# Performance work log

Hardware: AMD Instinct MI355X
Metric: run time of the kernel (lower is better)

## Reference

```python
import jax, jax.numpy as jnp
import numpy as np

N_KNOTS = 16
DEGREE = 3
N_BASES = N_KNOTS - DEGREE - 1  # 12
F_CH = 128
KNOTS = jnp.linspace(0.0, 2.0, N_KNOTS, dtype=jnp.float32)


def bspline_basis(x, knots, degree):
    """Cox-de Boor B-spline basis. x: [...], returns [..., K-degree-1]."""
    K = knots.shape[0]
    xe = x[..., None]
    # degree-0 indicator basis: [..., K-1]
    b = ((xe >= knots[:-1]) & (xe < knots[1:])).astype(x.dtype)
    for d in range(1, degree + 1):
        left_den = knots[d:K - 1] - knots[:K - d - 1]
        right_den = knots[d + 1:K] - knots[1:K - d]
        safe_l = jnp.where(left_den > 0, left_den, 1.0)
        safe_r = jnp.where(right_den > 0, right_den, 1.0)
        left = jnp.where(left_den > 0, (xe - knots[:K - d - 1]) / safe_l, 0.0)
        right = jnp.where(right_den > 0, (knots[d + 1:K] - xe) / safe_r, 0.0)
        b = left * b[..., :K - d - 1] + right * b[..., 1:K - d]
    return b  # [..., K-degree-1]


def setup_inputs() -> dict:
    key = jax.random.key(0)
    k1, k2, k3 = jax.random.split(key, 3)
    B, N = 32, 8192
    eval_x = jax.random.normal(k1, (B, N, F_CH), dtype=jnp.float32)
    eval_eigs = jax.random.uniform(k2, (B, N), dtype=jnp.float32)  # in [0,1) within knot span [0,2]
    filter_scale = 1.0
    filter_coeffs = jax.random.normal(k3, (N_BASES, F_CH), dtype=jnp.float32) * filter_scale
    return {"eval_x": eval_x, "eval_eigs": eval_eigs, "filter_coeffs": filter_coeffs}


def reference(eval_x, eval_eigs, filter_coeffs):
    # basis: [B, N, n_bases]
    basis = bspline_basis(eval_eigs, KNOTS, DEGREE)
    # The torch split/cat/bmm/stack/transpose chain is exactly this contraction:
    # spectral_filter[b,n,f] = sum_k basis[b,n,k] * coeffs[k,f]
    spectral_filter = jnp.einsum('bnk,kf->bnf', basis, filter_coeffs)
    return eval_x * jnp.square(spectral_filter)
```

## Files before the change

### kernel.cpp

```cpp
#include <hip/hip_runtime.h>


#define N_BASES 12
#define F_CH 128
#define CHUNKS 4
#define PAD 3
#define TAB_ROWS (N_BASES + 2 * PAD)
#define ROW_VF4 (F_CH / 4)

typedef float vf4 __attribute__((ext_vector_type(4)));

template <bool EXACT>
__global__ __launch_bounds__(256) void spline_filter_kernel(
    const vf4* __restrict__ x4,
    const float* __restrict__ eigs,
    const vf4* __restrict__ coeffs4,
    vf4*       __restrict__ out4,
    int total4, int stride4)
{
    __shared__ vf4 sc[TAB_ROWS * ROW_VF4];

    const int t = threadIdx.x;
    for (int r = t; r < TAB_ROWS * ROW_VF4; r += 256) {
        const int k = (r >> 5) - PAD;
        sc[r] = ((unsigned)k < (unsigned)N_BASES)
                    ? coeffs4[k * ROW_VF4 + (r & 31)]
                    : (vf4)0.0f;
    }
    __syncthreads();

    const int gid = blockIdx.x * 256 + t;

    float eg[CHUNKS];
    vf4   xv[CHUNKS];

    #pragma unroll
    for (int c = 0; c < CHUNKS; ++c) {
        const int idx = gid + c * stride4;
        if (EXACT || idx < total4) eg[c] = eigs[idx >> 5];
        else                       eg[c] = 0.0f;
    }
    #pragma unroll
    for (int c = 0; c < CHUNKS; ++c) {
        const int idx = gid + c * stride4;
        if (EXACT || idx < total4) xv[c] = __builtin_nontemporal_load(&x4[idx]);
        else                       xv[c] = (vf4)0.0f;
    }

    const int lane = gid & 31;

    #pragma unroll
    for (int c = 0; c < CHUNKS; ++c) {
        const int idx = gid + c * stride4;
        if (!EXACT && idx >= total4) continue;

        const float u = eg[c] * 7.5f;
        int i = (int)u;
        i = min(max(i, 0), N_BASES + 2);
        float tt = u - (float)i;
        tt = fminf(fmaxf(tt, 0.0f), 1.0f);
        const float t2  = tt * tt;
        const float t3  = t2 * tt;
        const float omt = 1.0f - tt;
        const float w0 = omt * omt * omt * (1.0f / 6.0f);
        const float w1 = (3.0f * t3 - 6.0f * t2 + 4.0f) * (1.0f / 6.0f);
        const float w2 = (-3.0f * t3 + 3.0f * t2 + 3.0f * tt + 1.0f) * (1.0f / 6.0f);
        const float w3 = t3 * (1.0f / 6.0f);

        const vf4* row = &sc[i * ROW_VF4 + lane];
        vf4 sf = w0 * row[0]
               + w1 * row[ROW_VF4]
               + w2 * row[2 * ROW_VF4]
               + w3 * row[3 * ROW_VF4];

        const vf4 o = xv[c] * sf * sf;
        __builtin_nontemporal_store(o, &out4[idx]);
    }
}

extern "C" void kernel_launch(void* const* d_in, const int* in_sizes, int n_in,
                              void* d_out, int out_size, void* d_ws, size_t ws_size,
                              hipStream_t stream) {
    const float* eval_x = (const float*)d_in[0];
    const float* eigs   = (const float*)d_in[1];
    const float* coeffs = (const float*)d_in[2];
    float* out = (float*)d_out;

    const int total4  = in_sizes[0] / 4;
    const int blocks  = (total4 + 256 * CHUNKS - 1) / (256 * CHUNKS);
    const int stride4 = blocks * 256;
    const bool exact  = (blocks * 256 * CHUNKS == total4);

    if (exact) {
        spline_filter_kernel<true><<<blocks, 256, 0, stream>>>(
            (const vf4*)eval_x, eigs, (const vf4*)coeffs, (vf4*)out,
            total4, stride4);
    } else {
        spline_filter_kernel<false><<<blocks, 256, 0, stream>>>(
            (const vf4*)eval_x, eigs, (const vf4*)coeffs, (vf4*)out,
            total4, stride4);
    }
}
```

Before: 227.9 us.

## Drop shared-memory coefficient table, read coefficients via cache with clamped indices

Removes the per-block shared-memory staging of the padded coefficient table and its barrier. Each thread now reads the four needed coefficient rows straight from global memory (served by L1/L2), clamping out-of-range basis indices and zeroing their weights. CHUNKS drops from 4 to 2, which doubles the block count, and launch bounds now request 8 blocks per CU for occupancy. The trade is more global/cache loads per element and less memory-level parallelism per thread, in exchange for no LDS setup or sync per block.

After: 226.1 us. Within noise of the previous version (-0.8%).

```diff
diff --git a/kernel.cpp b/kernel.cpp
--- a/kernel.cpp
+++ b/kernel.cpp
@@ -3,33 +3,20 @@
 
 #define N_BASES 12
 #define F_CH 128
-#define CHUNKS 4
-#define PAD 3
-#define TAB_ROWS (N_BASES + 2 * PAD)
+#define CHUNKS 2
 #define ROW_VF4 (F_CH / 4)
 
 typedef float vf4 __attribute__((ext_vector_type(4)));
 
 template <bool EXACT>
-__global__ __launch_bounds__(256) void spline_filter_kernel(
+__global__ __launch_bounds__(256, 8) void spline_filter_kernel(
     const vf4* __restrict__ x4,
     const float* __restrict__ eigs,
     const vf4* __restrict__ coeffs4,
     vf4*       __restrict__ out4,
     int total4, int stride4)
 {
-    __shared__ vf4 sc[TAB_ROWS * ROW_VF4];
-
-    const int t = threadIdx.x;
-    for (int r = t; r < TAB_ROWS * ROW_VF4; r += 256) {
-        const int k = (r >> 5) - PAD;
-        sc[r] = ((unsigned)k < (unsigned)N_BASES)
-                    ? coeffs4[k * ROW_VF4 + (r & 31)]
-                    : (vf4)0.0f;
-    }
-    __syncthreads();
-
-    const int gid = blockIdx.x * 256 + t;
+    const int gid = blockIdx.x * 256 + threadIdx.x;
 
     float eg[CHUNKS];
     vf4   xv[CHUNKS];
@@ -54,24 +41,27 @@
         const int idx = gid + c * stride4;
         if (!EXACT && idx >= total4) continue;
 
-        const float u = eg[c] * 7.5f;
-        int i = (int)u;
-        i = min(max(i, 0), N_BASES + 2);
-        float tt = u - (float)i;
-        tt = fminf(fmaxf(tt, 0.0f), 1.0f);
+        float u = eg[c] * 7.5f;
+        u = fminf(fmaxf(u, 0.0f), 15.0f);
+        const int   i  = (int)u;
+        const float tt = u - (float)i;
         const float t2  = tt * tt;
         const float t3  = t2 * tt;
         const float omt = 1.0f - tt;
-        const float w0 = omt * omt * omt * (1.0f / 6.0f);
-        const float w1 = (3.0f * t3 - 6.0f * t2 + 4.0f) * (1.0f / 6.0f);
-        const float w2 = (-3.0f * t3 + 3.0f * t2 + 3.0f * tt + 1.0f) * (1.0f / 6.0f);
-        const float w3 = t3 * (1.0f / 6.0f);
+        float w[4];
+        w[0] = omt * omt * omt * (1.0f / 6.0f);
+        w[1] = (3.0f * t3 - 6.0f * t2 + 4.0f) * (1.0f / 6.0f);
+        w[2] = (-3.0f * t3 + 3.0f * t2 + 3.0f * tt + 1.0f) * (1.0f / 6.0f);
+        w[3] = t3 * (1.0f / 6.0f);
 
-        const vf4* row = &sc[i * ROW_VF4 + lane];
-        vf4 sf = w0 * row[0]
-               + w1 * row[ROW_VF4]
-               + w2 * row[2 * ROW_VF4]
-               + w3 * row[3 * ROW_VF4];
+        vf4 sf = (vf4)0.0f;
+        #pragma unroll
+        for (int j = 0; j < 4; ++j) {
+            const int k  = i - 3 + j;
+            const int kc = min(max(k, 0), N_BASES - 1);
+            const float wj = (k == kc) ? w[j] : 0.0f;
+            sf += wj * coeffs4[kc * ROW_VF4 + lane];
+        }
 
         const vf4 o = xv[c] * sf * sf;
         __builtin_nontemporal_store(o, &out4[idx]);
```
